# Kernel tuning notes

Measured on AMD Instinct MI355X. Metric: run time of the kernel, lower is better.

The kernel has to match this reference:

```python
import jax, jax.numpy as jnp
import numpy as np

B, S, Q, I, A = 32, 2048, 1024, 1024, 1024


def setup_inputs() -> dict:
    key = jax.random.key(0)
    ks = jax.random.split(key, 6)
    return {
        "queries": jax.random.normal(ks[0], (B, 1, Q), dtype=jnp.float32),
        "multiple_items": jax.random.normal(ks[1], (B, S, I), dtype=jnp.float32),
        "weights": jax.random.randint(ks[2], (B, S), 0, 2, dtype=jnp.int32),
        # nn.Linear(in, out, bias=False) weights, stored as [in, out] for x @ W
        "W": jax.random.normal(ks[3], (Q, A), dtype=jnp.float32) / np.float32(np.sqrt(Q)),
        "U": jax.random.normal(ks[4], (I, A), dtype=jnp.float32) / np.float32(np.sqrt(I)),
        "v": jax.random.normal(ks[5], (A,), dtype=jnp.float32) / np.float32(np.sqrt(A)),
    }


def reference(queries, multiple_items, weights, W, U, v):
    # queries: [B,1,Q], multiple_items: [B,S,I], weights: [B,S] int mask
    pq = jnp.einsum('btq,qa->bta', queries, W)          # [B,1,A]
    pi = jnp.einsum('bsi,ia->bsa', multiple_items, U)   # [B,S,A]
    added = jnp.tanh(pq + pi)                           # [B,S,A] broadcast add
    reactivity = jnp.einsum('bsa,a->bs', added, v)      # [B,S]
    reactivity = jnp.where(weights == 0, -jnp.inf, reactivity)
    attention_scores = jax.nn.softmax(reactivity, axis=1)  # [B,S]
    blended = jnp.einsum('bs,bsi->bi', attention_scores, multiple_items)  # [B,I]
    return blended, attention_scores
```

## Files before the change

kernel.cpp:

```cpp
#include <hip/hip_runtime.h>
#include <hip/hip_bf16.h>
#include <cstdint>

#define BB 32
#define SS 2048
#define QQ 1024
#define II 1024
#define AA 1024
#define MM (BB * SS)

typedef __bf16 bf16x8 __attribute__((ext_vector_type(8)));
typedef float  f32x4  __attribute__((ext_vector_type(4)));

__device__ __forceinline__ unsigned int pack_bf2(float a, float b) {
  unsigned ua = __builtin_bit_cast(unsigned, a) + 0x8000u;
  unsigned ub = __builtin_bit_cast(unsigned, b) + 0x8000u;
  return __builtin_amdgcn_perm(ub, ua, 0x07060302u);
}

__device__ __forceinline__ void gload_lds16(const void* g, void* l) {
  __builtin_amdgcn_global_load_lds(
      (const __attribute__((address_space(1))) void*)g,
      (__attribute__((address_space(3))) void*)l, 16, 0, 0);
}

__global__ void __launch_bounds__(256) k_transpose_u(const float* __restrict__ U,
                                                     unsigned short* __restrict__ Ut) {
  __shared__ float t[64][65];
  const int n0 = blockIdx.x * 64, k0 = blockIdx.y * 64;
  const int c = threadIdx.x & 63, r0 = threadIdx.x >> 6;
#pragma unroll
  for (int r = r0; r < 64; r += 4) t[r][c] = U[(size_t)(k0 + r) * AA + n0 + c];
  __syncthreads();
#pragma unroll
  for (int r = r0; r < 64; r += 4) {
    __hip_bfloat16 h = __float2bfloat16(t[c][r]);
    Ut[(size_t)(n0 + r) * II + k0 + c] = __builtin_bit_cast(unsigned short, h);
  }
}

__global__ void __launch_bounds__(256) k_conv_swz(const float* __restrict__ in,
                                                  unsigned short* __restrict__ Aswz) {
  __shared__ unsigned short swz[16 * 1024];
  const int mt = blockIdx.x, tid = threadIdx.x;
  const float4* src = (const float4*)(in + (size_t)mt * 16 * 1024);
#pragma unroll
  for (int i = 0; i < 16; ++i) {
    const int e4 = i * 256 + tid;
    float4 f = src[e4];
    uint2 h;
    h.x = pack_bf2(f.x, f.y);
    h.y = pack_bf2(f.z, f.w);
    *(uint2*)&swz[e4 * 4] = h;
  }
  __syncthreads();
  uint4* dst = (uint4*)Aswz + (size_t)mt * 2048;
#pragma unroll
  for (int i = 0; i < 8; ++i) {
    const int s = i * 256 + tid;
    const int m = s & 15;
    const int lf = s & 63;
    const int quadk = lf >> 4;
    const int kc = s >> 6;
    const int e4b = m * 256 + kc * 8 + quadk * 2;
    uint2 lo = *(const uint2*)&swz[e4b * 4];
    uint2 hi = *(const uint2*)&swz[(e4b + 1) * 4];
    uint4 w; w.x = lo.x; w.y = lo.y; w.z = hi.x; w.w = hi.y;
    dst[s] = w;
  }
}

__global__ void __launch_bounds__(256) k_pq(const float* __restrict__ q,
                                            const float* __restrict__ W,
                                            float* __restrict__ pq) {
  __shared__ float qs[32 * 256];
  const int ab = blockIdx.x, qc = blockIdx.y, tid = threadIdx.x;
#pragma unroll
  for (int j = 0; j < 32; ++j) qs[j * 256 + tid] = q[j * QQ + qc * 256 + tid];
  __syncthreads();
  const int a  = ab * 128 + (tid & 127);
  const int bg = tid >> 7;
  float acc[16] = {};
  const float* Wp = W + (size_t)(qc * 256) * AA + a;
  for (int i = 0; i < 256; ++i) {
    const float w = Wp[(size_t)i * AA];
#pragma unroll
    for (int bb = 0; bb < 16; ++bb) acc[bb] += w * qs[(bg * 16 + bb) * 256 + i];
  }
#pragma unroll
  for (int bb = 0; bb < 16; ++bb) atomicAdd(&pq[(bg * 16 + bb) * AA + a], acc[bb]);
}

__device__ __forceinline__ void react_epilogue(f32x4 (&acc)[4][4], const float* pq,
                                               const float* v, float* react,
                                               int b, int m0, int n0, int wm, int wn,
                                               int quad, int sx) {
  float pqv[4], vv[4];
#pragma unroll
  for (int ni = 0; ni < 4; ++ni) {
    const int n = n0 + wn * 64 + ni * 16 + sx;
    pqv[ni] = pq[b * AA + n];
    vv[ni]  = v[n];
  }
#pragma unroll
  for (int mi = 0; mi < 4; ++mi) {
#pragma unroll
    for (int reg = 0; reg < 4; ++reg) {
      float ssum = 0.f;
#pragma unroll
      for (int ni = 0; ni < 4; ++ni) {
        const float x = acc[mi][ni][reg] + pqv[ni];
        const float e = __expf(2.f * x);
        const float t = 1.f - 2.f * __builtin_amdgcn_rcpf(e + 1.f);
        ssum += t * vv[ni];
      }
      ssum += __shfl_xor(ssum, 1);
      ssum += __shfl_xor(ssum, 2);
      ssum += __shfl_xor(ssum, 4);
      ssum += __shfl_xor(ssum, 8);
      if (sx == 0) {
        const int m = m0 + wm * 64 + mi * 16 + quad * 4 + reg;
        atomicAdd(&react[m], ssum);
      }
    }
  }
}

__global__ void __launch_bounds__(256, 3) k_gemm_bf(const unsigned short* __restrict__ Aswz,
                                                    const unsigned short* __restrict__ Ut,
                                                    const float* __restrict__ pq,
                                                    const float* __restrict__ v,
                                                    float* __restrict__ react) {
  __shared__ unsigned short Bs[128 * 64];

  const int tid  = threadIdx.x;
  const int lane = tid & 63, wid = tid >> 6;
  const int wm = wid >> 1, wn = wid & 1;
  const int quad = lane >> 4, sx = lane & 15;

  const unsigned id = blockIdx.x;
  const int xcd = id & 7;
  const int j   = id >> 3;
  const int mtile = xcd + 8 * (j >> 3);
  const int ntile = j & 7;
  const int m0 = mtile * 128, n0 = ntile * 128;
  const int b  = m0 >> 11;

  const int r_loc = lane >> 3;
  const int cch   = lane & 7;
  const int gch   = cch ^ r_loc;

  const bf16x8* Ab = (const bf16x8*)Aswz;
  const int m16b = (m0 + wm * 64) >> 4;

  f32x4 acc[4][4] = {};

  for (int kk = 0; kk < 16; ++kk) {
    const int k0 = kk * 64;
    __syncthreads();
#pragma unroll
    for (int jj = 0; jj < 4; ++jj) {
      const int rB = wid * 32 + jj * 8 + r_loc;
      gload_lds16(Ut + (size_t)(n0 + rB) * II + k0 + gch * 8,
                  &Bs[(wid * 32 + jj * 8) * 64]);
    }
    bf16x8 af[2][4];
#pragma unroll
    for (int ks = 0; ks < 2; ++ks) {
      const int g = kk * 2 + ks;
#pragma unroll
      for (int mi = 0; mi < 4; ++mi)
        af[ks][mi] = Ab[(size_t)((m16b + mi) * 32 + g) * 64 + lane];
    }
    __syncthreads();
#pragma unroll
    for (int ks = 0; ks < 2; ++ks) {
      bf16x8 bfv[4];
#pragma unroll
      for (int ni = 0; ni < 4; ++ni) {
        const int r = wn * 64 + ni * 16 + sx;
        const int c = (ks * 4 + quad) ^ (r & 7);
        bfv[ni] = *(const bf16x8*)&Bs[r * 64 + c * 8];
      }
#pragma unroll
      for (int mi = 0; mi < 4; ++mi)
#pragma unroll
        for (int ni = 0; ni < 4; ++ni)
          acc[mi][ni] = __builtin_amdgcn_mfma_f32_16x16x32_bf16(af[ks][mi], bfv[ni], acc[mi][ni], 0, 0, 0);
    }
  }
  react_epilogue(acc, pq, v, react, b, m0, n0, wm, wn, quad, sx);
}

__global__ void __launch_bounds__(256) k_gemm_f32(const float* __restrict__ items,
                                                  const unsigned short* __restrict__ Ut,
                                                  const float* __restrict__ pq,
                                                  const float* __restrict__ v,
                                                  float* __restrict__ react) {
  __shared__ unsigned short As[128 * 64];
  __shared__ unsigned short Bs[128 * 64];
  const int tid  = threadIdx.x;
  const int lane = tid & 63, wid = tid >> 6;
  const int wm = wid >> 1, wn = wid & 1;
  const int quad = lane >> 4, sx = lane & 15;
  const unsigned id = blockIdx.x;
  const int xcd = id & 7;
  const int j   = id >> 3;
  const int mtile = xcd + 8 * (j >> 3);
  const int ntile = j & 7;
  const int m0 = mtile * 128, n0 = ntile * 128;
  const int b  = m0 >> 11;
  const int ar = tid >> 2, aq = tid & 3;
  const int bn = tid >> 1, bh = tid & 1;
  f32x4 acc[4][4] = {};
  for (int kk = 0; kk < 16; ++kk) {
    const int k0 = kk * 64;
    __syncthreads();
#pragma unroll
    for (int rr = 0; rr < 2; ++rr) {
      const int r = ar + rr * 64;
      const float* g = items + (size_t)(m0 + r) * II + k0 + aq * 16;
      float4 f0 = ((const float4*)g)[0];
      float4 f1 = ((const float4*)g)[1];
      float4 f2 = ((const float4*)g)[2];
      float4 f3 = ((const float4*)g)[3];
      uint4 w0, w1;
      w0.x = pack_bf2(f0.x, f0.y); w0.y = pack_bf2(f0.z, f0.w);
      w0.z = pack_bf2(f1.x, f1.y); w0.w = pack_bf2(f1.z, f1.w);
      w1.x = pack_bf2(f2.x, f2.y); w1.y = pack_bf2(f2.z, f2.w);
      w1.z = pack_bf2(f3.x, f3.y); w1.w = pack_bf2(f3.z, f3.w);
      const int c0 = (2 * aq) ^ (r & 7);
      const int c1 = (2 * aq + 1) ^ (r & 7);
      *(uint4*)&As[r * 64 + c0 * 8] = w0;
      *(uint4*)&As[r * 64 + c1 * 8] = w1;
    }
    {
      const unsigned short* g = Ut + (size_t)(n0 + bn) * II + k0 + bh * 32;
#pragma unroll
      for (int jj = 0; jj < 4; ++jj) {
        uint4 w = ((const uint4*)g)[jj];
        const int c = (bh * 4 + jj) ^ (bn & 7);
        *(uint4*)&Bs[bn * 64 + c * 8] = w;
      }
    }
    __syncthreads();
#pragma unroll
    for (int ks = 0; ks < 2; ++ks) {
      bf16x8 af[4], bfv[4];
#pragma unroll
      for (int mi = 0; mi < 4; ++mi) {
        const int r = wm * 64 + mi * 16 + sx;
        const int c = (ks * 4 + quad) ^ (r & 7);
        af[mi] = *(const bf16x8*)&As[r * 64 + c * 8];
      }
#pragma unroll
      for (int ni = 0; ni < 4; ++ni) {
        const int r = wn * 64 + ni * 16 + sx;
        const int c = (ks * 4 + quad) ^ (r & 7);
        bfv[ni] = *(const bf16x8*)&Bs[r * 64 + c * 8];
      }
#pragma unroll
      for (int mi = 0; mi < 4; ++mi)
#pragma unroll
        for (int ni = 0; ni < 4; ++ni)
          acc[mi][ni] = __builtin_amdgcn_mfma_f32_16x16x32_bf16(af[mi], bfv[ni], acc[mi][ni], 0, 0, 0);
    }
  }
  react_epilogue(acc, pq, v, react, b, m0, n0, wm, wn, quad, sx);
}

__global__ void __launch_bounds__(256) k_softmax(const float* __restrict__ react,
                                                 const int* __restrict__ weights,
                                                 float* __restrict__ scores) {
  const int b = blockIdx.x, tid = threadIdx.x;
  const int lane = tid & 63, wid = tid >> 6;
  __shared__ float redm[4], reds[4];
  float vals[8];
  float mx = -3.0e38f;
#pragma unroll
  for (int j = 0; j < 8; ++j) {
    const int s = j * 256 + tid;
    const float r = react[b * SS + s];
    const int w = weights[b * SS + s];
    const float val = (w != 0) ? r : -3.0e38f;
    vals[j] = val;
    mx = fmaxf(mx, val);
  }
#pragma unroll
  for (int off = 1; off < 64; off <<= 1) mx = fmaxf(mx, __shfl_xor(mx, off));
  if (lane == 0) redm[wid] = mx;
  __syncthreads();
  mx = fmaxf(fmaxf(redm[0], redm[1]), fmaxf(redm[2], redm[3]));
  float e[8], sum = 0.f;
#pragma unroll
  for (int j = 0; j < 8; ++j) {
    e[j] = (vals[j] < -1.0e38f) ? 0.f : __expf(vals[j] - mx);
    sum += e[j];
  }
#pragma unroll
  for (int off = 1; off < 64; off <<= 1) sum += __shfl_xor(sum, off);
  if (lane == 0) reds[wid] = sum;
  __syncthreads();
  const float inv = 1.f / (reds[0] + reds[1] + reds[2] + reds[3]);
#pragma unroll
  for (int j = 0; j < 8; ++j) scores[b * SS + j * 256 + tid] = e[j] * inv;
}

__global__ void __launch_bounds__(256) k_blended(const float* __restrict__ items,
                                                 const float* __restrict__ scores,
                                                 float* __restrict__ out) {
  const int b = blockIdx.x, chunk = blockIdx.y, tid = threadIdx.x;
  __shared__ int   lidx[132];
  __shared__ float lsc[132];
  __shared__ int   lcount;
  if (tid == 0) lcount = 0;
  __syncthreads();
  if (tid < 128) {
    const int s = chunk * 128 + tid;
    const float sc = scores[b * SS + s];
    if (sc != 0.f) {
      const int p = atomicAdd(&lcount, 1);
      lidx[p] = s; lsc[p] = sc;
    }
  }
  __syncthreads();
  const int cnt = lcount;
  if (tid < 4) {
    const int p = cnt + tid;
    if (p < 132) { lidx[p] = chunk * 128; lsc[p] = 0.f; }
  }
  __syncthreads();
  const int cnt4 = (cnt + 3) & ~3;
  const float4* base = (const float4*)(items + (size_t)b * SS * II);
  float4 acc = {0.f, 0.f, 0.f, 0.f};
  for (int j0 = 0; j0 < cnt4; j0 += 4) {
    const int   s0 = lidx[j0],   s1 = lidx[j0+1], s2 = lidx[j0+2], s3 = lidx[j0+3];
    const float w0 = lsc[j0],    w1 = lsc[j0+1],  w2 = lsc[j0+2],  w3 = lsc[j0+3];
    const float4 x0 = base[(size_t)s0 * 256 + tid];
    const float4 x1 = base[(size_t)s1 * 256 + tid];
    const float4 x2 = base[(size_t)s2 * 256 + tid];
    const float4 x3 = base[(size_t)s3 * 256 + tid];
    acc.x += w0*x0.x + w1*x1.x + w2*x2.x + w3*x3.x;
    acc.y += w0*x0.y + w1*x1.y + w2*x2.y + w3*x3.y;
    acc.z += w0*x0.z + w1*x1.z + w2*x2.z + w3*x3.z;
    acc.w += w0*x0.w + w1*x1.w + w2*x2.w + w3*x3.w;
  }
  float* o = out + b * II + tid * 4;
  atomicAdd(o + 0, acc.x);
  atomicAdd(o + 1, acc.y);
  atomicAdd(o + 2, acc.z);
  atomicAdd(o + 3, acc.w);
}

extern "C" void kernel_launch(void* const* d_in, const int* in_sizes, int n_in,
                              void* d_out, int out_size, void* d_ws, size_t ws_size,
                              hipStream_t stream) {
  const float* queries = (const float*)d_in[0];
  const float* items   = (const float*)d_in[1];
  const int*   weights = (const int*)d_in[2];
  const float* W       = (const float*)d_in[3];
  const float* U       = (const float*)d_in[4];
  const float* v       = (const float*)d_in[5];
  float* out = (float*)d_out;

  char* ws = (char*)d_ws;
  unsigned short* Ut = (unsigned short*)ws;
  float* pq    = (float*)(ws + (2u << 20));
  float* react = (float*)(ws + (2u << 20) + (128u << 10));
  const size_t bf_off = (2u << 20) + (128u << 10) + (256u << 10);
  unsigned short* Aswz = (unsigned short*)(ws + bf_off);
  const bool pathA = ws_size >= bf_off + (size_t)MM * II * 2;

  hipMemsetAsync(pq, 0, BB * AA * sizeof(float), stream);
  hipMemsetAsync(react, 0, MM * sizeof(float), stream);
  hipMemsetAsync(out, 0, BB * II * sizeof(float), stream);

  k_transpose_u<<<dim3(16, 16), 256, 0, stream>>>(U, Ut);
  k_pq<<<dim3(8, 4), 256, 0, stream>>>(queries, W, pq);
  if (pathA) {
    k_conv_swz<<<dim3(4096), 256, 0, stream>>>(items, Aswz);
    k_gemm_bf<<<dim3(4096), 256, 0, stream>>>(Aswz, Ut, pq, v, react);
  } else {
    k_gemm_f32<<<dim3(4096), 256, 0, stream>>>(items, Ut, pq, v, react);
  }
  k_softmax<<<dim3(BB), 256, 0, stream>>>(react, weights, out + BB * II);
  k_blended<<<dim3(BB, 16), 256, 0, stream>>>(items, out + BB * II, out);
}
```

Baseline: 611.3 us.

## Double-buffer B tile and A fragments in bf16 GEMM, pad conversion LDS

The bf16 GEMM kernel now ping-pongs between two LDS buffers for the U tile and two register sets for A fragments, so the loads for the next k-step are issued before the MFMAs of the current step. This aims to hide global load latency behind compute, at the cost of doubled B LDS and extra VGPRs for A, which may reduce occupancy under launch_bounds(256,3). Separately, the conversion kernel pads its LDS rows to 1028 elements to cut bank conflicts on the strided reads.

```diff
diff --git a/kernel.cpp b/kernel.cpp
--- a/kernel.cpp
+++ b/kernel.cpp
@@ -39,19 +39,21 @@
   }
 }
 
+#define CRS 1028
 __global__ void __launch_bounds__(256) k_conv_swz(const float* __restrict__ in,
                                                   unsigned short* __restrict__ Aswz) {
-  __shared__ unsigned short swz[16 * 1024];
+  __shared__ unsigned short swz[16 * CRS];
   const int mt = blockIdx.x, tid = threadIdx.x;
   const float4* src = (const float4*)(in + (size_t)mt * 16 * 1024);
 #pragma unroll
   for (int i = 0; i < 16; ++i) {
     const int e4 = i * 256 + tid;
+    const int m = e4 >> 8, q = e4 & 255;
     float4 f = src[e4];
     uint2 h;
     h.x = pack_bf2(f.x, f.y);
     h.y = pack_bf2(f.z, f.w);
-    *(uint2*)&swz[e4 * 4] = h;
+    *(uint2*)&swz[m * CRS + q * 4] = h;
   }
   __syncthreads();
   uint4* dst = (uint4*)Aswz + (size_t)mt * 2048;
@@ -59,12 +61,11 @@
   for (int i = 0; i < 8; ++i) {
     const int s = i * 256 + tid;
     const int m = s & 15;
-    const int lf = s & 63;
-    const int quadk = lf >> 4;
+    const int quadk = (s & 63) >> 4;
     const int kc = s >> 6;
-    const int e4b = m * 256 + kc * 8 + quadk * 2;
-    uint2 lo = *(const uint2*)&swz[e4b * 4];
-    uint2 hi = *(const uint2*)&swz[(e4b + 1) * 4];
+    const int idx = m * CRS + kc * 32 + quadk * 8;
+    uint2 lo = *(const uint2*)&swz[idx];
+    uint2 hi = *(const uint2*)&swz[idx + 4];
     uint4 w; w.x = lo.x; w.y = lo.y; w.z = hi.x; w.w = hi.y;
     dst[s] = w;
   }
@@ -131,7 +132,8 @@
                                                     const float* __restrict__ pq,
                                                     const float* __restrict__ v,
                                                     float* __restrict__ react) {
-  __shared__ unsigned short Bs[128 * 64];
+  __shared__ unsigned short Bs0[128 * 64];
+  __shared__ unsigned short Bs1[128 * 64];
 
   const int tid  = threadIdx.x;
   const int lane = tid & 63, wid = tid >> 6;
@@ -154,42 +156,71 @@
   const int m16b = (m0 + wm * 64) >> 4;
 
   f32x4 acc[4][4] = {};
-
-  for (int kk = 0; kk < 16; ++kk) {
-    const int k0 = kk * 64;
+  bf16x8 afA[2][4], afB[2][4];
+
+#define ISSUE_B(BUF, KK)                                                        \
+  {                                                                             \
+    const int _k0 = (KK) * 64;                                                  \
+    _Pragma("unroll")                                                           \
+    for (int jj = 0; jj < 4; ++jj) {                                            \
+      const int rB = wid * 32 + jj * 8 + r_loc;                                 \
+      gload_lds16(Ut + (size_t)(n0 + rB) * II + _k0 + gch * 8,                  \
+                  &BUF[(wid * 32 + jj * 8) * 64]);                              \
+    }                                                                           \
+  }
+
+#define LOAD_A(AF, KK)                                                          \
+  {                                                                             \
+    _Pragma("unroll")                                                           \
+    for (int ks = 0; ks < 2; ++ks) {                                            \
+      const int g = (KK) * 2 + ks;                                              \
+      _Pragma("unroll")                                                         \
+      for (int mi = 0; mi < 4; ++mi)                                            \
+        AF[ks][mi] = Ab[(size_t)((m16b + mi) * 32 + g) * 64 + lane];            \
+    }                                                                           \
+  }
+
+#define GEMM_STEP(BUF, AF)                                                      \
+  {                                                                             \
+    _Pragma("unroll")                                                           \
+    for (int ks = 0; ks < 2; ++ks) {                                            \
+      bf16x8 bfv[4];                                                            \
+      _Pragma("unroll")                                                         \
+      for (int ni = 0; ni < 4; ++ni) {                                          \
+        const int r = wn * 64 + ni * 16 + sx;                                   \
+        const int c = (ks * 4 + quad) ^ (r & 7);                                \
+        bfv[ni] = *(const bf16x8*)&BUF[r * 64 + c * 8];                         \
+      }                                                                         \
+      _Pragma("unroll")                                                         \
+      for (int mi = 0; mi < 4; ++mi)                                            \
+        _Pragma("unroll")                                                       \
+        for (int ni = 0; ni < 4; ++ni)                                          \
+          acc[mi][ni] = __builtin_amdgcn_mfma_f32_16x16x32_bf16(                \
+              AF[ks][mi], bfv[ni], acc[mi][ni], 0, 0, 0);                       \
+    }                                                                           \
+  }
+
+  ISSUE_B(Bs0, 0);
+  LOAD_A(afA, 0);
+  __syncthreads();
+
+  for (int kk = 0; kk < 16; kk += 2) {
+    ISSUE_B(Bs1, kk + 1);
+    LOAD_A(afB, kk + 1);
+    GEMM_STEP(Bs0, afA);
     __syncthreads();
-#pragma unroll
-    for (int jj = 0; jj < 4; ++jj) {
-      const int rB = wid * 32 + jj * 8 + r_loc;
-      gload_lds16(Ut + (size_t)(n0 + rB) * II + k0 + gch * 8,
-                  &Bs[(wid * 32 + jj * 8) * 64]);
-    }
-    bf16x8 af[2][4];
-#pragma unroll
-    for (int ks = 0; ks < 2; ++ks) {
-      const int g = kk * 2 + ks;
-#pragma unroll
-      for (int mi = 0; mi < 4; ++mi)
-        af[ks][mi] = Ab[(size_t)((m16b + mi) * 32 + g) * 64 + lane];
-    }
+    if (kk + 2 < 16) {
+      ISSUE_B(Bs0, kk + 2);
+      LOAD_A(afA, kk + 2);
+    }
+    GEMM_STEP(Bs1, afB);
     __syncthreads();
-#pragma unroll
-    for (int ks = 0; ks < 2; ++ks) {
-      bf16x8 bfv[4];
-#pragma unroll
-      for (int ni = 0; ni < 4; ++ni) {
-        const int r = wn * 64 + ni * 16 + sx;
-        const int c = (ks * 4 + quad) ^ (r & 7);
-        bfv[ni] = *(const bf16x8*)&Bs[r * 64 + c * 8];
-      }
-#pragma unroll
-      for (int mi = 0; mi < 4; ++mi)
-#pragma unroll
-        for (int ni = 0; ni < 4; ++ni)
-          acc[mi][ni] = __builtin_amdgcn_mfma_f32_16x16x32_bf16(af[ks][mi], bfv[ni], acc[mi][ni], 0, 0, 0);
-    }
-  }
+  }
+
   react_epilogue(acc, pq, v, react, b, m0, n0, wm, wn, quad, sx);
+#undef ISSUE_B
+#undef LOAD_A
+#undef GEMM_STEP
 }
 
 __global__ void __launch_bounds__(256) k_gemm_f32(const float* __restrict__ items,
```

Result: slower. 653.4 us (+6.9%).
